# Kernel optimization log

Measured on AMD Instinct MI355X. Metric: run time of the kernel, lower is better.

## Reference

```python
import jax, jax.numpy as jnp
import numpy as np

LSTM_DIM = 2048
MEL_DIM = 512
INPUT_SIZE = 512
MAX_STEPS = 512
BATCH = 64


def setup_inputs() -> dict:
    key = jax.random.key(0)
    ks = jax.random.split(key, 9)
    s = 0.02
    return {
        "encoder_output": jax.random.normal(ks[0], (BATCH, 128, INPUT_SIZE), jnp.float32),
        "h0": jax.random.normal(ks[1], (1, BATCH, LSTM_DIM), jnp.float32),
        "c0": jax.random.normal(ks[2], (1, BATCH, LSTM_DIM), jnp.float32),
        "W_ih": jax.random.normal(ks[3], (4 * LSTM_DIM, INPUT_SIZE), jnp.float32) * s,
        "W_hh": jax.random.normal(ks[4], (4 * LSTM_DIM, LSTM_DIM), jnp.float32) * s,
        "b_ih": jax.random.normal(ks[5], (4 * LSTM_DIM,), jnp.float32) * s,
        "b_hh": jax.random.normal(ks[6], (4 * LSTM_DIM,), jnp.float32) * s,
        "W_out": jax.random.normal(ks[7], (MEL_DIM, LSTM_DIM), jnp.float32) * s,
        "b_out": jax.random.normal(ks[8], (MEL_DIM,), jnp.float32) * s,
    }


def reference(encoder_output, h0, c0, W_ih, W_hh, b_ih, b_hh, W_out, b_out):
    # never fires with random weights, so run MAX_STEPS via lax.scan.
    B = encoder_output.shape[0]
    h, c = h0[0], c0[0]                       # [B, H]
    x = jnp.zeros((B, MEL_DIM), encoder_output.dtype)  # initial decoder input
    bias = b_ih + b_hh

    def step(carry, _):
        x, h, c = carry
        gates = x @ W_ih.T + h @ W_hh.T + bias  # [B, 4H]
        i, f, g, o = jnp.split(gates, 4, axis=-1)  # torch gate order i,f,g,o
        c_new = jax.nn.sigmoid(f) * c + jax.nn.sigmoid(i) * jnp.tanh(g)
        h_new = jax.nn.sigmoid(o) * jnp.tanh(c_new)
        y = h_new @ W_out.T + b_out              # [B, mel]
        return (y, h_new, c_new), y

    _, ys = jax.lax.scan(step, (x, h, c), None, length=MAX_STEPS)  # [T, B, mel]
    return jnp.transpose(ys, (1, 0, 2))  # [B, T, mel]
```

## Files before the change

### kernel.cpp

```cpp
#include <hip/hip_runtime.h>

#define HDIM 2048
#define G4   8192
#define NB   64
#define NT   512
#define MEL  512
#define KIN  512
#define NWG  256
#define NBH  (NB * HDIM)
#define NSLOT 512

typedef __attribute__((ext_vector_type(8))) short short8;
typedef __attribute__((ext_vector_type(4))) float f32x4;
typedef __attribute__((ext_vector_type(4))) unsigned uint32x4;

__device__ __forceinline__ unsigned short f2bf(float f){
  union { float f; unsigned u; } v; v.f = f;
  return (unsigned short)((v.u + 0x7fffu + ((v.u >> 16) & 1u)) >> 16);
}
__device__ __forceinline__ float sigm(float x){ return 1.f / (1.f + __expf(-x)); }
__device__ __forceinline__ float tanhfast(float x){ return 1.f - 2.f / (__expf(2.f * x) + 1.f); }

__device__ __forceinline__ f32x4 MF(short8 a, short8 b, f32x4 c){
  return __builtin_amdgcn_mfma_f32_16x16x32_bf16(a, b, c, 0, 0, 0);
}
__device__ __forceinline__ short8 as8(uint32x4 u){
  union { uint32x4 u; short8 s; } x; x.u = u; return x.s;
}
template<bool RING>
__device__ __forceinline__ void ldh(uint32x4& d, const unsigned short* p){
  if constexpr (RING)
    asm volatile("global_load_dwordx4 %0, %1, off"
                 : "=&v"(d) : "v"(p) : "memory");
  else
    asm volatile("global_load_dwordx4 %0, %1, off sc0 sc1"
                 : "=&v"(d) : "v"(p) : "memory");
}

__global__ void convert_kernel(const float* __restrict__ src, unsigned short* __restrict__ dst, int n4){
  int stride = gridDim.x * blockDim.x;
  for (int i = blockIdx.x * blockDim.x + threadIdx.x; i < n4; i += stride){
    const float4 v = *(const float4*)(src + (size_t)i * 4);
    uint2 pk;
    pk.x = (unsigned)f2bf(v.x) | ((unsigned)f2bf(v.y) << 16);
    pk.y = (unsigned)f2bf(v.z) | ((unsigned)f2bf(v.w) << 16);
    *(uint2*)(dst + (size_t)i * 4) = pk;
  }
}

__global__ void beff_kernel(const float* __restrict__ W_ih, const float* __restrict__ b_ih,
                            const float* __restrict__ b_hh, const float* __restrict__ b_out,
                            float* __restrict__ b_eff){
  int r = blockIdx.x;
  int lane = threadIdx.x;
  float acc = 0.f;
  for (int k = lane; k < KIN; k += 64) acc += W_ih[(size_t)r * KIN + k] * b_out[k];
  #pragma unroll
  for (int off = 32; off > 0; off >>= 1) acc += __shfl_down(acc, off, 64);
  if (lane == 0) b_eff[r] = b_ih[r] + b_hh[r] + acc;
}

__global__ void ym1_kernel(const float* __restrict__ Wout, const float* __restrict__ h0,
                           const float* __restrict__ b_out, float* __restrict__ ym1){
  const int b = blockIdx.x;
  const int m = blockIdx.y * 64 + threadIdx.x;
  const float* wr = Wout + (size_t)m * HDIM;
  const float* hr = h0 + (size_t)b * HDIM;
  float a0 = 0.f, a1 = 0.f, a2 = 0.f, a3 = 0.f;
  for (int k = 0; k < HDIM; k += 4){
    const float4 wv = *(const float4*)(wr + k);
    const float4 hv = *(const float4*)(hr + k);
    a0 += wv.x * hv.x; a1 += wv.y * hv.y; a2 += wv.z * hv.z; a3 += wv.w * hv.w;
  }
  ym1[(size_t)b * MEL + m] = a0 + a1 + a2 + a3 + b_out[m];
}

__global__ void corr_kernel(const float* __restrict__ Wih, const float* __restrict__ ym1,
                            float* __restrict__ corr){
  const int r = blockIdx.x;
  const int b = threadIdx.x;
  const float* wr = Wih + (size_t)r * KIN;
  const float* yr = ym1 + (size_t)b * MEL;
  float a0 = 0.f, a1 = 0.f, a2 = 0.f, a3 = 0.f;
  for (int m = 0; m < KIN; m += 4){
    const float4 wv = *(const float4*)(wr + m);
    const float4 yv = *(const float4*)(yr + m);
    a0 += wv.x * yv.x; a1 += wv.y * yv.y; a2 += wv.z * yv.z; a3 += wv.w * yv.w;
  }
  corr[(size_t)r * NB + b] = a0 + a1 + a2 + a3;
}

__global__ __launch_bounds__(256) void weff_gemm(const float* __restrict__ W_ih, const float* __restrict__ W_out,
                                                 const float* __restrict__ W_hh, unsigned short* __restrict__ Weff){
  __shared__ __align__(16) float As[32][68];
  __shared__ __align__(16) float Bs[32][68];
  const int bn = blockIdx.x * 64;
  const int bm = blockIdx.y * 64;
  const int t = threadIdx.x;
  const int tx = t & 15, ty = t >> 4;
  float acc[4][4] = {};
  for (int k0 = 0; k0 < KIN; k0 += 32){
    #pragma unroll
    for (int i = 0; i < 2; i++){
      int f = t + i * 256;
      int row = f >> 3, c4 = (f & 7) * 4;
      const float4 v = *(const float4*)(W_ih + (size_t)(bm + row) * KIN + k0 + c4);
      As[c4 + 0][row] = v.x; As[c4 + 1][row] = v.y; As[c4 + 2][row] = v.z; As[c4 + 3][row] = v.w;
    }
    #pragma unroll
    for (int i = 0; i < 2; i++){
      int f = t + i * 256;
      int kr = f >> 4, c4 = (f & 15) * 4;
      *(float4*)&Bs[kr][c4] = *(const float4*)(W_out + (size_t)(k0 + kr) * HDIM + bn + c4);
    }
    __syncthreads();
    #pragma unroll
    for (int kk = 0; kk < 32; kk++){
      const float4 av = *(const float4*)&As[kk][ty * 4];
      const float4 bv = *(const float4*)&Bs[kk][tx * 4];
      const float ar[4] = {av.x, av.y, av.z, av.w};
      const float br[4] = {bv.x, bv.y, bv.z, bv.w};
      #pragma unroll
      for (int i = 0; i < 4; i++)
        #pragma unroll
        for (int j = 0; j < 4; j++)
          acc[i][j] += ar[i] * br[j];
    }
    __syncthreads();
  }
  #pragma unroll
  for (int i = 0; i < 4; i++){
    const size_t row = (size_t)bm + ty * 4 + i;
    const float4 wh = *(const float4*)(W_hh + row * HDIM + bn + tx * 4);
    uint2 pk;
    pk.x = (unsigned)f2bf(acc[i][0] + wh.x) | ((unsigned)f2bf(acc[i][1] + wh.y) << 16);
    pk.y = (unsigned)f2bf(acc[i][2] + wh.z) | ((unsigned)f2bf(acc[i][3] + wh.w) << 16);
    *(uint2*)(Weff + row * HDIM + bn + tx * 4) = pk;
  }
}

__device__ __forceinline__ void wait64(const unsigned* __restrict__ base, int lane, unsigned tgt){
  const unsigned* sp = base + lane;
  while (true){
    unsigned vv;
    asm volatile("global_load_dword %0, %1, off sc0 sc1\n\t"
                 "s_waitcnt vmcnt(0)"
                 : "=v"(vv) : "v"(sp) : "memory");
    if (__all((int)(vv >= tgt))) break;
    __builtin_amdgcn_s_sleep(1);
  }
}

#define LDSX (16384*4 + 512*4)

template<bool RING>
__global__ void __launch_bounds__(512, 1) decoder_coop(
    const unsigned short* __restrict__ Weff_b,
    const unsigned short* __restrict__ Wout_b,
    const float* __restrict__ b_eff,
    const float* __restrict__ corr,
    const float* __restrict__ c0,
    const float* __restrict__ b_out,
    unsigned short* __restrict__ hring,
    unsigned* __restrict__ slots,
    float* __restrict__ out)
{
  extern __shared__ char smem[];
  float* exf = (float*)smem;
  float* eyf = exf + 16384;
  const int bid  = blockIdx.x;
  const int d    = bid & 1;
  const int jg   = bid >> 1;
  const int tid  = threadIdx.x;
  const int v    = tid >> 6;
  const int lane = tid & 63;
  const int col  = lane & 15;
  const int q    = lane >> 4;
  const int kbase = v * 256;

  short8 A0[8], A1[8], A2[8], A3[8], Ay[8];
  #pragma unroll
  for (int it = 0; it < 8; ++it){
    const size_t kc = (size_t)kbase + it * 32 + q * 8;
    A0[it] = *(const short8*)(Weff_b + (size_t)(0 * HDIM + jg * 16 + col) * HDIM + kc);
    A1[it] = *(const short8*)(Weff_b + (size_t)(1 * HDIM + jg * 16 + col) * HDIM + kc);
    A2[it] = *(const short8*)(Weff_b + (size_t)(2 * HDIM + jg * 16 + col) * HDIM + kc);
    A3[it] = *(const short8*)(Weff_b + (size_t)(3 * HDIM + jg * 16 + col) * HDIM + kc);
    if (col < 4)
      Ay[it] = *(const short8*)(Wout_b + (size_t)(jg * 4 + col) * HDIM + kc);
    else { short8 z = {0,0,0,0,0,0,0,0}; Ay[it] = z; }
  }

  const int jl = tid & 15;
  const int bs = tid >> 4;
  const int rj = jg * 16 + jl;
  float be0 = 0.f, be1 = 0.f, be2 = 0.f, be3 = 0.f;
  float cs_s0 = 0.f, cs_s1 = 0.f;
  if (tid < 256){
    be0 = b_eff[0 * HDIM + rj]; be1 = b_eff[1 * HDIM + rj];
    be2 = b_eff[2 * HDIM + rj]; be3 = b_eff[3 * HDIM + rj];
    cs_s0 = c0[(size_t)(d * 32 + bs) * HDIM + rj];
    cs_s1 = c0[(size_t)(d * 32 + 16 + bs) * HDIM + rj];
  }
  const bool isY = (tid >= 256 && tid < 320);
  float byo = 0.f; int yr = 0, ybs = 0;
  if (isY){ const int yt = tid - 256; yr = yt & 3; ybs = yt >> 2; byo = b_out[jg * 4 + yr]; }

  int boff[2];
  #pragma unroll
  for (int s = 0; s < 2; ++s)
    boff[s] = (d * 32 + s * 16 + col) * HDIM + kbase + q * 8;

#define WAITV(N) asm volatile("s_waitcnt vmcnt(" #N ")" ::: "memory"); __builtin_amdgcn_sched_barrier(0);
#define MFM(IT, G) { \
    const short8 bv = as8(G); \
    a0 = MF(A0[IT], bv, a0); a1 = MF(A1[IT], bv, a1); \
    a2 = MF(A2[IT], bv, a2); a3 = MF(A3[IT], bv, a3); \
    ay = MF(Ay[IT], bv, ay); }

  for (int t = 0; t < NT; ++t){
    #pragma unroll
    for (int s = 0; s < 2; ++s){
      unsigned* slot_ds = slots + (d * 2 + s) * NSLOT;
      if (t) wait64(slot_ds + 64 * v, lane, (unsigned)t);

      const unsigned short* hcur = hring + (size_t)(RING ? t : (t & 1)) * NBH;
      const int bo = boff[s];
      uint32x4 G0, G1, G2, G3;
      f32x4 a0 = {0,0,0,0}, a1 = {0,0,0,0}, a2 = {0,0,0,0}, a3 = {0,0,0,0}, ay = {0,0,0,0};

      ldh<RING>(G0, hcur + bo);
      ldh<RING>(G1, hcur + bo + 32);
      ldh<RING>(G2, hcur + bo + 64);
      ldh<RING>(G3, hcur + bo + 96);
      WAITV(3) MFM(0, G0) ldh<RING>(G0, hcur + bo + 128);
      WAITV(3) MFM(1, G1) ldh<RING>(G1, hcur + bo + 160);
      WAITV(3) MFM(2, G2) ldh<RING>(G2, hcur + bo + 192);
      WAITV(3) MFM(3, G3) ldh<RING>(G3, hcur + bo + 224);
      WAITV(3) MFM(4, G0)
      WAITV(2) MFM(5, G1)
      WAITV(1) MFM(6, G2)
      WAITV(0) MFM(7, G3)

      __syncthreads();

      #pragma unroll
      for (int e = 0; e < 4; ++e){
        const int lr = q * 4 + e;
        const int cx = col ^ ((lr & 7) << 2);
        exf[(v * 64 +  0 + lr) * 32 + cx] = a0[e];
        exf[(v * 64 + 16 + lr) * 32 + cx] = a1[e];
        exf[(v * 64 + 32 + lr) * 32 + cx] = a2[e];
        exf[(v * 64 + 48 + lr) * 32 + cx] = a3[e];
      }
      if (q == 0){
        #pragma unroll
        for (int e = 0; e < 4; ++e) eyf[(v * 4 + e) * 16 + col] = ay[e];
      }
      __syncthreads();

      if (tid < 256){
        const int cidx = bs ^ ((jl & 7) << 2);
        float gi = 0.f, gf = 0.f, gg = 0.f, go = 0.f;
        #pragma unroll
        for (int vv = 0; vv < 8; ++vv){
          gi += exf[(vv * 64 +  0 + jl) * 32 + cidx];
          gf += exf[(vv * 64 + 16 + jl) * 32 + cidx];
          gg += exf[(vv * 64 + 32 + jl) * 32 + cidx];
          go += exf[(vv * 64 + 48 + jl) * 32 + cidx];
        }
        const int b = d * 32 + s * 16 + bs;
        gi += be0; gf += be1; gg += be2; go += be3;
        if (t == 0){
          gi -= corr[(size_t)(0 * HDIM + rj) * NB + b];
          gf -= corr[(size_t)(1 * HDIM + rj) * NB + b];
          gg -= corr[(size_t)(2 * HDIM + rj) * NB + b];
          go -= corr[(size_t)(3 * HDIM + rj) * NB + b];
        }
        float cs = s ? cs_s1 : cs_s0;
        const float i_ = sigm(gi), f_ = sigm(gf), g_ = tanhfast(gg), o_ = sigm(go);
        cs = f_ * cs + i_ * g_;
        const float hn = o_ * tanhfast(cs);
        if (s) cs_s1 = cs; else cs_s0 = cs;

        const float pn = __shfl_xor(hn, 1, 64);
        unsigned short* hdst = hring + (size_t)(RING ? (t + 1) : ((t + 1) & 1)) * NBH;
        if ((jl & 1) == 0){
          const unsigned pk = (unsigned)f2bf(hn) | ((unsigned)f2bf(pn) << 16);
          __hip_atomic_store((unsigned*)(hdst + (size_t)b * HDIM + rj), pk,
                             __ATOMIC_RELAXED, __HIP_MEMORY_SCOPE_AGENT);
        }
        asm volatile("s_waitcnt vmcnt(0)" ::: "memory");
        __builtin_amdgcn_sched_barrier(0);
        if (lane == 0)
          __hip_atomic_store(slot_ds + (jg << 2) + v, (unsigned)(t + 1),
                             __ATOMIC_RELAXED, __HIP_MEMORY_SCOPE_AGENT);
      } else if (isY && t >= 1){
        float yv = byo;
        #pragma unroll
        for (int vv = 0; vv < 8; ++vv) yv += eyf[(vv * 4 + yr) * 16 + ybs];
        const int b = d * 32 + s * 16 + ybs;
        out[((size_t)b * NT + (t - 1)) * MEL + jg * 4 + yr] = yv;
      }
    }
  }

  #pragma unroll
  for (int s = 0; s < 2; ++s){
    wait64(slots + (d * 2 + s) * NSLOT + 64 * v, lane, (unsigned)NT);
    const unsigned short* hfin = hring + (size_t)(RING ? NT : 0) * NBH;
    const int bo = boff[s];
    f32x4 ay = {0,0,0,0};
    #pragma unroll
    for (int it = 0; it < 8; ++it){
      uint32x4 g;
      ldh<RING>(g, hfin + bo + it * 32);
      asm volatile("s_waitcnt vmcnt(0)" ::: "memory");
      __builtin_amdgcn_sched_barrier(0);
      ay = MF(Ay[it], as8(g), ay);
    }
    __syncthreads();
    if (q == 0){
      #pragma unroll
      for (int e = 0; e < 4; ++e) eyf[(v * 4 + e) * 16 + col] = ay[e];
    }
    __syncthreads();
    if (isY){
      float yv = byo;
      #pragma unroll
      for (int vv = 0; vv < 8; ++vv) yv += eyf[(vv * 4 + yr) * 16 + ybs];
      const int b = d * 32 + s * 16 + ybs;
      out[((size_t)b * NT + 511) * MEL + jg * 4 + yr] = yv;
    }
    __syncthreads();
  }
}

extern "C" void kernel_launch(void* const* d_in, const int* in_sizes, int n_in,
                              void* d_out, int out_size, void* d_ws, size_t ws_size,
                              hipStream_t stream){
  (void)in_sizes; (void)n_in; (void)out_size;
  const float* h0    = (const float*)d_in[1];
  const float* c0    = (const float*)d_in[2];
  const float* W_ih  = (const float*)d_in[3];
  const float* W_hh  = (const float*)d_in[4];
  const float* b_ih  = (const float*)d_in[5];
  const float* b_hh  = (const float*)d_in[6];
  const float* W_out = (const float*)d_in[7];
  const float* b_out = (const float*)d_in[8];
  float* out = (float*)d_out;

  const size_t fixed = (size_t)G4 * HDIM * 2
                     + (size_t)MEL * HDIM * 2
                     + (size_t)G4 * 4
                     + (size_t)G4 * NB * 4
                     + (size_t)NB * MEL * 4
                     + 4 * NSLOT * sizeof(unsigned)
                     + 1024;
  const bool ring = ws_size >= fixed + (size_t)(NT + 1) * NBH * 2;
  const int hslots = ring ? (NT + 1) : 2;

  char* p = (char*)d_ws;
  unsigned short* weff_b = (unsigned short*)p; p += (size_t)G4 * HDIM * 2;
  unsigned short* wout_b = (unsigned short*)p; p += (size_t)MEL * HDIM * 2;
  float* beff = (float*)p;  p += (size_t)G4 * 4;
  float* corr = (float*)p;  p += (size_t)G4 * NB * 4;
  float* ym1  = (float*)p;  p += (size_t)NB * MEL * 4;
  unsigned* slots = (unsigned*)p; p += 4 * NSLOT * sizeof(unsigned);
  unsigned short* hring = (unsigned short*)p; p += (size_t)hslots * NBH * 2;

  hipMemsetAsync(slots, 0, 4 * NSLOT * sizeof(unsigned), stream);
  convert_kernel<<<256, 256, 0, stream>>>(W_out, wout_b, MEL * HDIM / 4);
  convert_kernel<<<64, 256, 0, stream>>>(h0, hring, NBH / 4);
  beff_kernel<<<G4, 64, 0, stream>>>(W_ih, b_ih, b_hh, b_out, beff);
  ym1_kernel<<<dim3(NB, MEL / 64), 64, 0, stream>>>(W_out, h0, b_out, ym1);
  corr_kernel<<<G4, NB, 0, stream>>>(W_ih, ym1, corr);
  weff_gemm<<<dim3(HDIM / 64, G4 / 64), 256, 0, stream>>>(W_ih, W_out, W_hh, weff_b);

  void* kargs[] = { (void*)&weff_b, (void*)&wout_b, (void*)&beff, (void*)&corr,
                    (void*)&c0, (void*)&b_out, (void*)&hring, (void*)&slots, (void*)&out };
  if (ring){
    hipFuncSetAttribute((const void*)decoder_coop<true>,
                        hipFuncAttributeMaxDynamicSharedMemorySize, LDSX);
    hipLaunchCooperativeKernel((const void*)decoder_coop<true>, dim3(NWG), dim3(512),
                               kargs, LDSX, stream);
  } else {
    hipFuncSetAttribute((const void*)decoder_coop<false>,
                        hipFuncAttributeMaxDynamicSharedMemorySize, LDSX);
    hipLaunchCooperativeKernel((const void*)decoder_coop<false>, dim3(NWG), dim3(512),
                               kargs, LDSX, stream);
  }
}
```

Baseline: 3.816 ms.

## Double-buffer LDS exchange per batch half and deepen h-load prefetch

```diff
diff --git a/kernel.cpp b/kernel.cpp
--- a/kernel.cpp
+++ b/kernel.cpp
@@ -9,6 +9,7 @@
 #define NWG  256
 #define NBH  (NB * HDIM)
 #define NSLOT 512
+#define EXBUF 16896
 
 typedef __attribute__((ext_vector_type(8))) short short8;
 typedef __attribute__((ext_vector_type(4))) float f32x4;
@@ -151,7 +152,7 @@
   }
 }
 
-#define LDSX (16384*4 + 512*4)
+#define LDSX (2 * EXBUF * 4)
 
 template<bool RING>
 __global__ void __launch_bounds__(512, 1) decoder_coop(
@@ -166,8 +167,6 @@
     float* __restrict__ out)
 {
   extern __shared__ char smem[];
-  float* exf = (float*)smem;
-  float* eyf = exf + 16384;
   const int bid  = blockIdx.x;
   const int d    = bid & 1;
   const int jg   = bid >> 1;
@@ -222,27 +221,29 @@
     #pragma unroll
     for (int s = 0; s < 2; ++s){
       unsigned* slot_ds = slots + (d * 2 + s) * NSLOT;
+      float* exf = (float*)smem + s * EXBUF;
+      float* eyf = exf + 16384;
       if (t) wait64(slot_ds + 64 * v, lane, (unsigned)t);
 
       const unsigned short* hcur = hring + (size_t)(RING ? t : (t & 1)) * NBH;
       const int bo = boff[s];
-      uint32x4 G0, G1, G2, G3;
+      uint32x4 P0, P1, P2, P3, P4, P5;
       f32x4 a0 = {0,0,0,0}, a1 = {0,0,0,0}, a2 = {0,0,0,0}, a3 = {0,0,0,0}, ay = {0,0,0,0};
 
-      ldh<RING>(G0, hcur + bo);
-      ldh<RING>(G1, hcur + bo + 32);
-      ldh<RING>(G2, hcur + bo + 64);
-      ldh<RING>(G3, hcur + bo + 96);
-      WAITV(3) MFM(0, G0) ldh<RING>(G0, hcur + bo + 128);
-      WAITV(3) MFM(1, G1) ldh<RING>(G1, hcur + bo + 160);
-      WAITV(3) MFM(2, G2) ldh<RING>(G2, hcur + bo + 192);
-      WAITV(3) MFM(3, G3) ldh<RING>(G3, hcur + bo + 224);
-      WAITV(3) MFM(4, G0)
-      WAITV(2) MFM(5, G1)
-      WAITV(1) MFM(6, G2)
-      WAITV(0) MFM(7, G3)
-
-      __syncthreads();
+      ldh<RING>(P0, hcur + bo);
+      ldh<RING>(P1, hcur + bo + 32);
+      ldh<RING>(P2, hcur + bo + 64);
+      ldh<RING>(P3, hcur + bo + 96);
+      ldh<RING>(P4, hcur + bo + 128);
+      ldh<RING>(P5, hcur + bo + 160);
+      WAITV(5) MFM(0, P0) ldh<RING>(P0, hcur + bo + 192);
+      WAITV(5) MFM(1, P1) ldh<RING>(P1, hcur + bo + 224);
+      WAITV(5) MFM(2, P2)
+      WAITV(4) MFM(3, P3)
+      WAITV(3) MFM(4, P4)
+      WAITV(2) MFM(5, P5)
+      WAITV(1) MFM(6, P0)
+      WAITV(0) MFM(7, P1)
 
       #pragma unroll
       for (int e = 0; e < 4; ++e){
@@ -308,6 +309,8 @@
   #pragma unroll
   for (int s = 0; s < 2; ++s){
     wait64(slots + (d * 2 + s) * NSLOT + 64 * v, lane, (unsigned)NT);
+    float* exf = (float*)smem + s * EXBUF;
+    float* eyf = exf + 16384;
     const unsigned short* hfin = hring + (size_t)(RING ? NT : 0) * NBH;
     const int bo = boff[s];
     f32x4 ay = {0,0,0,0};
```

Measured after the change: 4.898 ms. +28.4%, slower.
